# Kernel tuning notes

Measured on AMD Instinct MI355X. Metric: run time of the kernel, lower is better.

Reference implementation:

```python
import jax, jax.numpy as jnp
import numpy as np

B, D, H, K, V, M = 64, 4096, 32, 128, 128, 4096


def setup_inputs() -> dict:
    key = jax.random.key(0)
    ks = jax.random.split(key, 7)
    return {
        "x": jax.random.normal(ks[0], (B, D), dtype=jnp.float32),
        "prev_K": jax.random.normal(ks[1], (B, M, K), dtype=jnp.float32),
        "prev_V": jax.random.normal(ks[2], (B, M, V), dtype=jnp.float32),
        "P_q": jax.random.normal(ks[3], (H, D, K), dtype=jnp.float32),
        "P_k": jax.random.normal(ks[4], (D, K), dtype=jnp.float32),
        "P_v": jax.random.normal(ks[5], (D, V), dtype=jnp.float32),
        "P_o": jax.random.normal(ks[6], (H, D, V), dtype=jnp.float32),
    }


def reference(x, prev_K, prev_V, P_q, P_k, P_v, P_o):
    # Per-head query projection: [b,d] x [h,d,k] -> [b,h,k]
    q = jnp.einsum('bd,hdk->bhk', x, P_q)
    # Single shared K/V head (multi-query): append new token to cache along m
    new_k = jnp.einsum('bd,dk->bk', x, P_k)  # [b,k]
    new_v = jnp.einsum('bd,dv->bv', x, P_v)  # [b,v]
    Kc = jnp.concatenate([prev_K, new_k[:, None, :]], axis=1)  # [b,m+1,k]
    Vc = jnp.concatenate([prev_V, new_v[:, None, :]], axis=1)  # [b,m+1,v]
    # Attention over cache
    logits = jnp.einsum('bhk,bmk->bhm', q, Kc)
    weights = jax.nn.softmax(logits, axis=-1)
    O = jnp.einsum('bhm,bmv->bhv', weights, Vc)
    # Output projection: [b,h,v] x [h,d,v] -> [b,d]
    y = jnp.einsum('bhv,hdv->bd', O, P_o)
    return (y, Kc, Vc)
```

## Files before the change

### kernel.cpp

```cpp
#include <hip/hip_runtime.h>
#include <math.h>

#define Bb 64
#define Dd 4096
#define Hh 32
#define Kk 128
#define Vv 128
#define Mm 4096
#define MC 4097
#define NCH 16
#define NSLOT 17

#define WS_K1P  0
#define WS_Q    4456448
#define WS_NEWK (WS_Q + Bb*Hh*Kk)
#define WS_NEWV (WS_NEWK + Bb*Kk)
#define WS_PM   (WS_NEWV + Bb*Vv)
#define WS_PL   (WS_PM + Bb*NSLOT*Hh)
#define WS_PO   (WS_PL + Bb*NSLOT*Hh)
#define WS_O    (WS_PO + Bb*NSLOT*Hh*Vv)
#define WS_YP   (WS_O + Bb*Hh*Vv)

#define YSLOT (Bb*Dd)

#define OUT_Y  0
#define OUT_KC (Bb*Dd)
#define OUT_VC (OUT_KC + Bb*MC*Kk)

__global__ __launch_bounds__(256) void k1A_proj(const float* __restrict__ x,
        const float* __restrict__ Pq, const float* __restrict__ Pk,
        const float* __restrict__ Pv, float* __restrict__ part) {
    const int hidx = blockIdx.x;
    const int d0c  = blockIdx.y * 256;
    const int t = threadIdx.x;
    const int kg = t & 15, bg = t >> 4;
    const int kd = kg * 4, b0 = bg * 4;

    const float* P;
    if (hidx < Hh)       P = Pq + (size_t)hidx * Dd * Kk;
    else if (hidx == Hh) P = Pk;
    else                 P = Pv;

    __shared__ float xs[32 * 65];
    __shared__ float ps[32 * 128];

    float acc[4][8];
    #pragma unroll
    for (int a = 0; a < 4; a++)
        #pragma unroll
        for (int c = 0; c < 8; c++) acc[a][c] = 0.f;

    for (int tt = 0; tt < 8; tt++) {
        const int d0 = d0c + tt * 32;
        #pragma unroll
        for (int ii = 0; ii < 8; ii++) {
            int f = ii * 256 + t;
            int i = f & 31, bb = f >> 5;
            xs[i * 65 + bb] = x[(size_t)bb * Dd + d0 + i];
        }
        #pragma unroll
        for (int ii = 0; ii < 4; ii++) {
            int f = ii * 256 + t;
            int i = f >> 5, k4 = (f & 31) * 4;
            *(float4*)&ps[i * 128 + k4] = *(const float4*)&P[(size_t)(d0 + i) * Kk + k4];
        }
        __syncthreads();
        #pragma unroll
        for (int i = 0; i < 32; i++) {
            float xb[4];
            #pragma unroll
            for (int a = 0; a < 4; a++) xb[a] = xs[i * 65 + b0 + a];
            float4 p0 = *(float4*)&ps[i * 128 + kd];
            float4 p1 = *(float4*)&ps[i * 128 + 64 + kd];
            float pp[8] = {p0.x, p0.y, p0.z, p0.w, p1.x, p1.y, p1.z, p1.w};
            #pragma unroll
            for (int a = 0; a < 4; a++)
                #pragma unroll
                for (int c = 0; c < 8; c++)
                    acc[a][c] = fmaf(xb[a], pp[c], acc[a][c]);
        }
        __syncthreads();
    }
    float* dst = part + ((size_t)hidx * 16 + blockIdx.y) * 8192;
    #pragma unroll
    for (int a = 0; a < 4; a++) {
        int b = b0 + a;
        *(float4*)&dst[b * 128 + kd]      = make_float4(acc[a][0], acc[a][1], acc[a][2], acc[a][3]);
        *(float4*)&dst[b * 128 + 64 + kd] = make_float4(acc[a][4], acc[a][5], acc[a][6], acc[a][7]);
    }
}

__global__ __launch_bounds__(256) void k1B_reduce(const float* __restrict__ part,
        float* __restrict__ ws) {
    const int o = blockIdx.x * 256 + threadIdx.x;
    const int hidx = o >> 13;
    const int rest = o & 8191;
    float s = 0.f;
    #pragma unroll
    for (int c = 0; c < 16; c++) s += part[((size_t)hidx * 16 + c) * 8192 + rest];
    if (hidx < Hh) {
        int b = rest >> 7, k = rest & 127;
        ws[WS_Q + ((size_t)b * Hh + hidx) * Kk + k] = s;
    } else if (hidx == Hh) {
        ws[WS_NEWK + rest] = s;
    } else {
        ws[WS_NEWV + rest] = s;
    }
}

__global__ __launch_bounds__(256) void kflash(const float* __restrict__ prevK,
        const float* __restrict__ prevV, const float* __restrict__ wq,
        float* __restrict__ outKc, float* __restrict__ outVc,
        float* __restrict__ PM, float* __restrict__ PL, float* __restrict__ PO) {
    const int c = blockIdx.x;
    const int b = blockIdx.y;
    const int t = threadIdx.x;
    const int hg = t >> 4, lg = t & 15;
    const int h2 = hg * 2;

    __shared__ float ks_t[64 * 64];
    __shared__ float vs[64 * 132];
    __shared__ float qs[128 * 34];
    __shared__ float wl_t[64 * 36];

    {
        const int h = t >> 3, kc = t & 7;
        const float* qr = wq + ((size_t)b * Hh + h) * Kk + kc * 16;
        float4 a0 = *(const float4*)&qr[0];
        float4 a1 = *(const float4*)&qr[4];
        float4 a2 = *(const float4*)&qr[8];
        float4 a3 = *(const float4*)&qr[12];
        const int k0 = kc * 16;
        qs[(k0+ 0)*34 + h] = a0.x; qs[(k0+ 1)*34 + h] = a0.y;
        qs[(k0+ 2)*34 + h] = a0.z; qs[(k0+ 3)*34 + h] = a0.w;
        qs[(k0+ 4)*34 + h] = a1.x; qs[(k0+ 5)*34 + h] = a1.y;
        qs[(k0+ 6)*34 + h] = a1.z; qs[(k0+ 7)*34 + h] = a1.w;
        qs[(k0+ 8)*34 + h] = a2.x; qs[(k0+ 9)*34 + h] = a2.y;
        qs[(k0+10)*34 + h] = a2.z; qs[(k0+11)*34 + h] = a2.w;
        qs[(k0+12)*34 + h] = a3.x; qs[(k0+13)*34 + h] = a3.y;
        qs[(k0+14)*34 + h] = a3.z; qs[(k0+15)*34 + h] = a3.w;
    }

    float rm[2] = {-3.0e38f, -3.0e38f};
    float rl[2] = {0.f, 0.f};
    float accO[2][8] = {};
    const int kq = t & 15;
    const int vq = t & 31;

    for (int st = 0; st < 4; st++) {
        const int m0 = c * 256 + st * 64;
        __syncthreads();
        float4 kreg[8], vreg[8];
        #pragma unroll
        for (int ii = 0; ii < 4; ii++) {
            int mm = (t >> 4) + ii * 16;
            const float* src = prevK + ((size_t)b * Mm + m0 + mm) * Kk + kq * 4;
            kreg[ii]     = *(const float4*)src;
            kreg[ii + 4] = *(const float4*)(src + 64);
        }
        #pragma unroll
        for (int ii = 0; ii < 8; ii++) {
            int mm = (t >> 5) + ii * 8;
            vreg[ii] = *(const float4*)(prevV + ((size_t)b * Mm + m0 + mm) * Vv + vq * 4);
        }
        #pragma unroll
        for (int ii = 0; ii < 4; ii++) {
            int mm = (t >> 4) + ii * 16;
            int cs = (mm + 4 * kq) & 63;
            ks_t[(kq*4+0)*64 + cs] = kreg[ii].x;
            ks_t[(kq*4+1)*64 + cs] = kreg[ii].y;
            ks_t[(kq*4+2)*64 + cs] = kreg[ii].z;
            ks_t[(kq*4+3)*64 + cs] = kreg[ii].w;
        }
        #pragma unroll
        for (int ii = 0; ii < 8; ii++) {
            int mm = (t >> 5) + ii * 8;
            *(float4*)&vs[mm * 132 + vq * 4] = vreg[ii];
        }
        __syncthreads();
        #pragma unroll
        for (int ii = 0; ii < 4; ii++) {
            int mm = (t >> 4) + ii * 16;
            float* dstK = outKc + ((size_t)b * MC + m0 + mm) * Kk + kq * 4;
            *(float4*)dstK        = kreg[ii];
            *(float4*)(dstK + 64) = kreg[ii + 4];
        }
        #pragma unroll
        for (int ii = 0; ii < 8; ii++) {
            int mm = (t >> 5) + ii * 8;
            *(float4*)(outVc + ((size_t)b * MC + m0 + mm) * Vv + vq * 4) = vreg[ii];
        }
        float s[2][4] = {};
        #pragma unroll 4
        for (int k = 0; k < 64; k++) {
            float2 q2 = *(float2*)&qs[k * 34 + h2];
            float4 k4 = *(float4*)&ks_t[k * 64 + ((4*lg + 4*(k>>2)) & 63)];
            s[0][0] = fmaf(q2.x, k4.x, s[0][0]); s[0][1] = fmaf(q2.x, k4.y, s[0][1]);
            s[0][2] = fmaf(q2.x, k4.z, s[0][2]); s[0][3] = fmaf(q2.x, k4.w, s[0][3]);
            s[1][0] = fmaf(q2.y, k4.x, s[1][0]); s[1][1] = fmaf(q2.y, k4.y, s[1][1]);
            s[1][2] = fmaf(q2.y, k4.z, s[1][2]); s[1][3] = fmaf(q2.y, k4.w, s[1][3]);
        }
        __syncthreads();
        #pragma unroll
        for (int ii = 0; ii < 4; ii++) {
            int mm = (t >> 4) + ii * 16;
            int cs = (mm + 4 * kq) & 63;
            ks_t[(kq*4+0)*64 + cs] = kreg[ii+4].x;
            ks_t[(kq*4+1)*64 + cs] = kreg[ii+4].y;
            ks_t[(kq*4+2)*64 + cs] = kreg[ii+4].z;
            ks_t[(kq*4+3)*64 + cs] = kreg[ii+4].w;
        }
        __syncthreads();
        #pragma unroll 4
        for (int k = 0; k < 64; k++) {
            float2 q2 = *(float2*)&qs[(64 + k) * 34 + h2];
            float4 k4 = *(float4*)&ks_t[k * 64 + ((4*lg + 4*(k>>2)) & 63)];
            s[0][0] = fmaf(q2.x, k4.x, s[0][0]); s[0][1] = fmaf(q2.x, k4.y, s[0][1]);
            s[0][2] = fmaf(q2.x, k4.z, s[0][2]); s[0][3] = fmaf(q2.x, k4.w, s[0][3]);
            s[1][0] = fmaf(q2.y, k4.x, s[1][0]); s[1][1] = fmaf(q2.y, k4.y, s[1][1]);
            s[1][2] = fmaf(q2.y, k4.z, s[1][2]); s[1][3] = fmaf(q2.y, k4.w, s[1][3]);
        }
        float al[2];
        #pragma unroll
        for (int a = 0; a < 2; a++) {
            float mloc = fmaxf(fmaxf(s[a][0], s[a][1]), fmaxf(s[a][2], s[a][3]));
            mloc = fmaxf(mloc, __shfl_xor(mloc, 1, 64));
            mloc = fmaxf(mloc, __shfl_xor(mloc, 2, 64));
            mloc = fmaxf(mloc, __shfl_xor(mloc, 4, 64));
            mloc = fmaxf(mloc, __shfl_xor(mloc, 8, 64));
            float nm = fmaxf(rm[a], mloc);
            al[a] = __expf(rm[a] - nm);
            float psum = 0.f;
            #pragma unroll
            for (int cc = 0; cc < 4; cc++) {
                float p = __expf(s[a][cc] - nm);
                wl_t[(4*lg + cc) * 36 + h2 + a] = p;
                psum += p;
            }
            psum += __shfl_xor(psum, 1, 64);
            psum += __shfl_xor(psum, 2, 64);
            psum += __shfl_xor(psum, 4, 64);
            psum += __shfl_xor(psum, 8, 64);
            rl[a] = rl[a] * al[a] + psum;
            rm[a] = nm;
        }
        #pragma unroll
        for (int a = 0; a < 2; a++)
            #pragma unroll
            for (int j = 0; j < 8; j++) accO[a][j] *= al[a];
        for (int mm = 0; mm < 64; mm++) {
            float2 w2 = *(float2*)&wl_t[mm * 36 + h2];
            float4 v0 = *(float4*)&vs[mm * 132 + 4 * lg];
            float4 v1 = *(float4*)&vs[mm * 132 + 64 + 4 * lg];
            accO[0][0] = fmaf(w2.x, v0.x, accO[0][0]);
            accO[0][1] = fmaf(w2.x, v0.y, accO[0][1]);
            accO[0][2] = fmaf(w2.x, v0.z, accO[0][2]);
            accO[0][3] = fmaf(w2.x, v0.w, accO[0][3]);
            accO[0][4] = fmaf(w2.x, v1.x, accO[0][4]);
            accO[0][5] = fmaf(w2.x, v1.y, accO[0][5]);
            accO[0][6] = fmaf(w2.x, v1.z, accO[0][6]);
            accO[0][7] = fmaf(w2.x, v1.w, accO[0][7]);
            accO[1][0] = fmaf(w2.y, v0.x, accO[1][0]);
            accO[1][1] = fmaf(w2.y, v0.y, accO[1][1]);
            accO[1][2] = fmaf(w2.y, v0.z, accO[1][2]);
            accO[1][3] = fmaf(w2.y, v0.w, accO[1][3]);
            accO[1][4] = fmaf(w2.y, v1.x, accO[1][4]);
            accO[1][5] = fmaf(w2.y, v1.y, accO[1][5]);
            accO[1][6] = fmaf(w2.y, v1.z, accO[1][6]);
            accO[1][7] = fmaf(w2.y, v1.w, accO[1][7]);
        }
    }
    const size_t base = ((size_t)b * NSLOT + c) * Hh;
    if (lg == 0) {
        PM[base + h2]     = rm[0];
        PM[base + h2 + 1] = rm[1];
        PL[base + h2]     = rl[0];
        PL[base + h2 + 1] = rl[1];
    }
    #pragma unroll
    for (int a = 0; a < 2; a++) {
        float* po = PO + (base + h2 + a) * Vv;
        *(float4*)&po[4*lg]      = make_float4(accO[a][0], accO[a][1], accO[a][2], accO[a][3]);
        *(float4*)&po[64 + 4*lg] = make_float4(accO[a][4], accO[a][5], accO[a][6], accO[a][7]);
    }
}

__global__ __launch_bounds__(128) void knew(const float* __restrict__ ws,
        float* __restrict__ outKc, float* __restrict__ outVc,
        float* __restrict__ PM, float* __restrict__ PL, float* __restrict__ PO) {
    const int b = blockIdx.x, t = threadIdx.x;
    const float* q    = ws + WS_Q;
    const float* newk = ws + WS_NEWK;
    const float* newv = ws + WS_NEWV;
    const int h = t >> 2, j = t & 3;
    const float* qr = q + ((size_t)b * Hh + h) * Kk + j * 32;
    const float* nk = newk + (size_t)b * Kk + j * 32;
    float s0 = 0.f, s1 = 0.f, s2 = 0.f, s3 = 0.f;
    #pragma unroll
    for (int i = 0; i < 8; i++) {
        float4 a  = *(const float4*)&qr[i * 4];
        float4 c4 = *(const float4*)&nk[i * 4];
        s0 = fmaf(a.x, c4.x, s0); s1 = fmaf(a.y, c4.y, s1);
        s2 = fmaf(a.z, c4.z, s2); s3 = fmaf(a.w, c4.w, s3);
    }
    float s = (s0 + s1) + (s2 + s3);
    s += __shfl_xor(s, 1, 64);
    s += __shfl_xor(s, 2, 64);
    const size_t base = ((size_t)b * NSLOT + 16) * Hh;
    if (j == 0) { PM[base + h] = s; PL[base + h] = 1.f; }
    float nv = newv[(size_t)b * Vv + t];
    outKc[((size_t)b * MC + Mm) * Kk + t] = newk[(size_t)b * Kk + t];
    outVc[((size_t)b * MC + Mm) * Vv + t] = nv;
    #pragma unroll 4
    for (int hh = 0; hh < Hh; hh++)
        PO[(base + hh) * Vv + t] = nv;
}

__global__ __launch_bounds__(128) void kcomb(const float* __restrict__ PM,
        const float* __restrict__ PL, const float* __restrict__ PO,
        float* __restrict__ O) {
    const int h = blockIdx.x, b = blockIdx.y, t = threadIdx.x;
    __shared__ float ml[NSLOT], ll[NSLOT];
    if (t < NSLOT) {
        ml[t] = PM[((size_t)b * NSLOT + t) * Hh + h];
        ll[t] = PL[((size_t)b * NSLOT + t) * Hh + h];
    }
    __syncthreads();
    float M = -3.0e38f;
    #pragma unroll
    for (int c = 0; c < NSLOT; c++) M = fmaxf(M, ml[c]);
    float L = 0.f, o = 0.f;
    #pragma unroll
    for (int c = 0; c < NSLOT; c++) {
        float e = __expf(ml[c] - M);
        L += ll[c] * e;
        o = fmaf(e, PO[(((size_t)b * NSLOT + c) * Hh + h) * Vv + t], o);
    }
    O[((size_t)b * Hh + h) * Vv + t] = o / L;
}

__global__ __launch_bounds__(256) void k5_outproj(const float* __restrict__ O,
        const float* __restrict__ Po, float* __restrict__ ypart) {
    const int dbase = blockIdx.x * 64;
    const int hq = blockIdx.y;
    const int t = threadIdx.x;
    __shared__ float os[64 * 64];
    __shared__ float ps2[64 * 64];
    const int dg = t & 15, bg = t >> 4;
    const int d0 = dg * 4, b0 = bg * 4;
    float acc[4][4] = {};
    for (int hi = 0; hi < 4; hi++) {
        const int h = hq * 4 + hi;
        for (int vh = 0; vh < 2; vh++) {
            __syncthreads();
            #pragma unroll
            for (int ii = 0; ii < 4; ii++) {
                int f = ii * 256 + t;
                int vq2 = f & 15, r = f >> 4;
                int colp = (4 * vq2 + 4 * (r >> 2)) & 63;
                *(float4*)&os[r * 64 + colp] =
                    *(const float4*)&O[((size_t)(r * Hh + h)) * Vv + vh * 64 + 4 * vq2];
                *(float4*)&ps2[r * 64 + colp] =
                    *(const float4*)&Po[((size_t)h * Dd + dbase + r) * Vv + vh * 64 + 4 * vq2];
            }
            __syncthreads();
            #pragma unroll
            for (int v4 = 0; v4 < 16; v4++) {
                float4 pd[4], ob[4];
                #pragma unroll
                for (int cc = 0; cc < 4; cc++)
                    pd[cc] = *(float4*)&ps2[(d0 + cc) * 64 + ((4*v4 + 4*dg) & 63)];
                #pragma unroll
                for (int a = 0; a < 4; a++)
                    ob[a] = *(float4*)&os[(b0 + a) * 64 + ((4*v4 + 4*bg) & 63)];
                #pragma unroll
                for (int a = 0; a < 4; a++)
                    #pragma unroll
                    for (int cc = 0; cc < 4; cc++) {
                        acc[a][cc] = fmaf(ob[a].x, pd[cc].x, acc[a][cc]);
                        acc[a][cc] = fmaf(ob[a].y, pd[cc].y, acc[a][cc]);
                        acc[a][cc] = fmaf(ob[a].z, pd[cc].z, acc[a][cc]);
                        acc[a][cc] = fmaf(ob[a].w, pd[cc].w, acc[a][cc]);
                    }
            }
        }
    }
    float* yp = ypart + (size_t)hq * YSLOT;
    #pragma unroll
    for (int a = 0; a < 4; a++)
        *(float4*)&yp[(size_t)(b0 + a) * Dd + dbase + d0] =
            make_float4(acc[a][0], acc[a][1], acc[a][2], acc[a][3]);
}

__global__ __launch_bounds__(256) void k5r_yreduce(const float* __restrict__ ypart,
        float* __restrict__ y) {
    const int o = blockIdx.x * 256 + threadIdx.x;
    float s = 0.f;
    #pragma unroll
    for (int c = 0; c < 8; c++) s += ypart[(size_t)c * YSLOT + o];
    y[o] = s;
}

extern "C" void kernel_launch(void* const* d_in, const int* in_sizes, int n_in,
                              void* d_out, int out_size, void* d_ws, size_t ws_size,
                              hipStream_t stream) {
    const float* x     = (const float*)d_in[0];
    const float* prevK = (const float*)d_in[1];
    const float* prevV = (const float*)d_in[2];
    const float* Pq    = (const float*)d_in[3];
    const float* Pk    = (const float*)d_in[4];
    const float* Pv    = (const float*)d_in[5];
    const float* Po    = (const float*)d_in[6];
    float* out = (float*)d_out;
    float* ws  = (float*)d_ws;

    k1A_proj<<<dim3(Hh + 2, 16), 256, 0, stream>>>(x, Pq, Pk, Pv, ws + WS_K1P);
    k1B_reduce<<<(34 * 8192) / 256, 256, 0, stream>>>(ws + WS_K1P, ws);
    kflash<<<dim3(NCH, Bb), 256, 0, stream>>>(prevK, prevV, ws + WS_Q,
                                              out + OUT_KC, out + OUT_VC,
                                              ws + WS_PM, ws + WS_PL, ws + WS_PO);
    knew<<<Bb, 128, 0, stream>>>(ws, out + OUT_KC, out + OUT_VC,
                                 ws + WS_PM, ws + WS_PL, ws + WS_PO);
    kcomb<<<dim3(Hh, Bb), 128, 0, stream>>>(ws + WS_PM, ws + WS_PL, ws + WS_PO,
                                            ws + WS_O);
    k5_outproj<<<dim3(64, 8), 256, 0, stream>>>(ws + WS_O, Po, ws + WS_YP);
    k5r_yreduce<<<YSLOT / 256, 256, 0, stream>>>(ws + WS_YP, out + OUT_Y);
}
```

Measured before the change: 252.9 us.

## Halve LDS footprint in flash kernel to raise occupancy, stage Q from registers

```diff
diff --git a/kernel.cpp b/kernel.cpp
--- a/kernel.cpp
+++ b/kernel.cpp
@@ -27,6 +27,13 @@
 #define OUT_KC (Bb*Dd)
 #define OUT_VC (OUT_KC + Bb*MC*Kk)
 
+#define BAR_LGKM() do { \
+    __builtin_amdgcn_sched_barrier(0); \
+    asm volatile("s_waitcnt lgkmcnt(0)" ::: "memory"); \
+    __builtin_amdgcn_s_barrier(); \
+    __builtin_amdgcn_sched_barrier(0); \
+} while (0)
+
 __global__ __launch_bounds__(256) void k1A_proj(const float* __restrict__ x,
         const float* __restrict__ Pq, const float* __restrict__ Pk,
         const float* __restrict__ Pv, float* __restrict__ part) {
@@ -108,7 +115,7 @@
     }
 }
 
-__global__ __launch_bounds__(256) void kflash(const float* __restrict__ prevK,
+__global__ __launch_bounds__(256, 3) void kflash(const float* __restrict__ prevK,
         const float* __restrict__ prevV, const float* __restrict__ wq,
         float* __restrict__ outKc, float* __restrict__ outVc,
         float* __restrict__ PM, float* __restrict__ PL, float* __restrict__ PO) {
@@ -117,80 +124,76 @@
     const int t = threadIdx.x;
     const int hg = t >> 4, lg = t & 15;
     const int h2 = hg * 2;
+    const int kq = t & 15;
+    const int mK = t >> 4;
+    const int vq = t & 31;
+    const int mV = t >> 5;
 
     __shared__ float ks_t[64 * 64];
-    __shared__ float vs[64 * 132];
-    __shared__ float qs[128 * 34];
+    __shared__ float vs[32 * 132];
+    __shared__ float qs[64 * 34];
     __shared__ float wl_t[64 * 36];
 
-    {
-        const int h = t >> 3, kc = t & 7;
-        const float* qr = wq + ((size_t)b * Hh + h) * Kk + kc * 16;
-        float4 a0 = *(const float4*)&qr[0];
-        float4 a1 = *(const float4*)&qr[4];
-        float4 a2 = *(const float4*)&qr[8];
-        float4 a3 = *(const float4*)&qr[12];
-        const int k0 = kc * 16;
-        qs[(k0+ 0)*34 + h] = a0.x; qs[(k0+ 1)*34 + h] = a0.y;
-        qs[(k0+ 2)*34 + h] = a0.z; qs[(k0+ 3)*34 + h] = a0.w;
-        qs[(k0+ 4)*34 + h] = a1.x; qs[(k0+ 5)*34 + h] = a1.y;
-        qs[(k0+ 6)*34 + h] = a1.z; qs[(k0+ 7)*34 + h] = a1.w;
-        qs[(k0+ 8)*34 + h] = a2.x; qs[(k0+ 9)*34 + h] = a2.y;
-        qs[(k0+10)*34 + h] = a2.z; qs[(k0+11)*34 + h] = a2.w;
-        qs[(k0+12)*34 + h] = a3.x; qs[(k0+13)*34 + h] = a3.y;
-        qs[(k0+14)*34 + h] = a3.z; qs[(k0+15)*34 + h] = a3.w;
-    }
+    float4 qreg[2][2];
+    #pragma unroll
+    for (int hf = 0; hf < 2; hf++)
+        #pragma unroll
+        for (int a = 0; a < 2; a++)
+            qreg[hf][a] = *(const float4*)&wq[((size_t)b * Hh + h2 + a) * Kk + hf * 64 + lg * 4];
 
     float rm[2] = {-3.0e38f, -3.0e38f};
     float rl[2] = {0.f, 0.f};
     float accO[2][8] = {};
-    const int kq = t & 15;
-    const int vq = t & 31;
 
     for (int st = 0; st < 4; st++) {
         const int m0 = c * 256 + st * 64;
-        __syncthreads();
-        float4 kreg[8], vreg[8];
+        BAR_LGKM();
+        float4 ka[8], va[8];
         #pragma unroll
         for (int ii = 0; ii < 4; ii++) {
-            int mm = (t >> 4) + ii * 16;
+            int mm = mK + ii * 16;
             const float* src = prevK + ((size_t)b * Mm + m0 + mm) * Kk + kq * 4;
-            kreg[ii]     = *(const float4*)src;
-            kreg[ii + 4] = *(const float4*)(src + 64);
+            ka[ii]     = *(const float4*)src;
+            ka[ii + 4] = *(const float4*)(src + 64);
         }
         #pragma unroll
         for (int ii = 0; ii < 8; ii++) {
-            int mm = (t >> 5) + ii * 8;
-            vreg[ii] = *(const float4*)(prevV + ((size_t)b * Mm + m0 + mm) * Vv + vq * 4);
-        }
+            int mm = mV + ii * 8;
+            va[ii] = *(const float4*)(prevV + ((size_t)b * Mm + m0 + mm) * Vv + vq * 4);
+        }
+        #pragma unroll
+        for (int ii = 0; ii < 4; ii++)
+            *(float4*)&vs[(mV + ii * 8) * 132 + vq * 4] = va[ii];
         #pragma unroll
         for (int ii = 0; ii < 4; ii++) {
-            int mm = (t >> 4) + ii * 16;
+            int mm = mK + ii * 16;
             int cs = (mm + 4 * kq) & 63;
-            ks_t[(kq*4+0)*64 + cs] = kreg[ii].x;
-            ks_t[(kq*4+1)*64 + cs] = kreg[ii].y;
-            ks_t[(kq*4+2)*64 + cs] = kreg[ii].z;
-            ks_t[(kq*4+3)*64 + cs] = kreg[ii].w;
+            ks_t[(kq*4+0)*64 + cs] = ka[ii].x;
+            ks_t[(kq*4+1)*64 + cs] = ka[ii].y;
+            ks_t[(kq*4+2)*64 + cs] = ka[ii].z;
+            ks_t[(kq*4+3)*64 + cs] = ka[ii].w;
+        }
+        {
+            float q0[4] = {qreg[0][0].x, qreg[0][0].y, qreg[0][0].z, qreg[0][0].w};
+            float q1[4] = {qreg[0][1].x, qreg[0][1].y, qreg[0][1].z, qreg[0][1].w};
+            #pragma unroll
+            for (int j = 0; j < 4; j++)
+                *(float2*)&qs[(lg * 4 + j) * 34 + h2] = make_float2(q0[j], q1[j]);
+        }
+        BAR_LGKM();
+        #pragma unroll
+        for (int ii = 0; ii < 4; ii++) {
+            int mm = mK + ii * 16;
+            float* dK = outKc + ((size_t)b * MC + m0 + mm) * Kk + kq * 4;
+            *(float4*)dK        = ka[ii];
+            *(float4*)(dK + 64) = ka[ii + 4];
         }
         #pragma unroll
         for (int ii = 0; ii < 8; ii++) {
-            int mm = (t >> 5) + ii * 8;
-            *(float4*)&vs[mm * 132 + vq * 4] = vreg[ii];
-        }
-        __syncthreads();
-        #pragma unroll
-        for (int ii = 0; ii < 4; ii++) {
-            int mm = (t >> 4) + ii * 16;
-            float* dstK = outKc + ((size_t)b * MC + m0 + mm) * Kk + kq * 4;
-            *(float4*)dstK        = kreg[ii];
-            *(float4*)(dstK + 64) = kreg[ii + 4];
-        }
-        #pragma unroll
-        for (int ii = 0; ii < 8; ii++) {
-            int mm = (t >> 5) + ii * 8;
-            *(float4*)(outVc + ((size_t)b * MC + m0 + mm) * Vv + vq * 4) = vreg[ii];
-        }
-        float s[2][4] = {};
+            int mm = mV + ii * 8;
+            *(float4*)(outVc + ((size_t)b * MC + m0 + mm) * Vv + vq * 4) = va[ii];
+        }
+        float s[2][4] = {{0.f,0.f,0.f,0.f},{0.f,0.f,0.f,0.f}};
         #pragma unroll 4
         for (int k = 0; k < 64; k++) {
             float2 q2 = *(float2*)&qs[k * 34 + h2];
@@ -200,20 +203,27 @@
             s[1][0] = fmaf(q2.y, k4.x, s[1][0]); s[1][1] = fmaf(q2.y, k4.y, s[1][1]);
             s[1][2] = fmaf(q2.y, k4.z, s[1][2]); s[1][3] = fmaf(q2.y, k4.w, s[1][3]);
         }
-        __syncthreads();
+        BAR_LGKM();
         #pragma unroll
         for (int ii = 0; ii < 4; ii++) {
-            int mm = (t >> 4) + ii * 16;
+            int mm = mK + ii * 16;
             int cs = (mm + 4 * kq) & 63;
-            ks_t[(kq*4+0)*64 + cs] = kreg[ii+4].x;
-            ks_t[(kq*4+1)*64 + cs] = kreg[ii+4].y;
-            ks_t[(kq*4+2)*64 + cs] = kreg[ii+4].z;
-            ks_t[(kq*4+3)*64 + cs] = kreg[ii+4].w;
-        }
-        __syncthreads();
+            ks_t[(kq*4+0)*64 + cs] = ka[ii+4].x;
+            ks_t[(kq*4+1)*64 + cs] = ka[ii+4].y;
+            ks_t[(kq*4+2)*64 + cs] = ka[ii+4].z;
+            ks_t[(kq*4+3)*64 + cs] = ka[ii+4].w;
+        }
+        {
+            float q0[4] = {qreg[1][0].x, qreg[1][0].y, qreg[1][0].z, qreg[1][0].w};
+            float q1[4] = {qreg[1][1].x, qreg[1][1].y, qreg[1][1].z, qreg[1][1].w};
+            #pragma unroll
+            for (int j = 0; j < 4; j++)
+                *(float2*)&qs[(lg * 4 + j) * 34 + h2] = make_float2(q0[j], q1[j]);
+        }
+        BAR_LGKM();
         #pragma unroll 4
         for (int k = 0; k < 64; k++) {
-            float2 q2 = *(float2*)&qs[(64 + k) * 34 + h2];
+            float2 q2 = *(float2*)&qs[k * 34 + h2];
             float4 k4 = *(float4*)&ks_t[k * 64 + ((4*lg + 4*(k>>2)) & 63)];
             s[0][0] = fmaf(q2.x, k4.x, s[0][0]); s[0][1] = fmaf(q2.x, k4.y, s[0][1]);
             s[0][2] = fmaf(q2.x, k4.z, s[0][2]); s[0][3] = fmaf(q2.x, k4.w, s[0][3]);
@@ -248,7 +258,8 @@
         for (int a = 0; a < 2; a++)
             #pragma unroll
             for (int j = 0; j < 8; j++) accO[a][j] *= al[a];
-        for (int mm = 0; mm < 64; mm++) {
+        #pragma unroll 4
+        for (int mm = 0; mm < 32; mm++) {
             float2 w2 = *(float2*)&wl_t[mm * 36 + h2];
             float4 v0 = *(float4*)&vs[mm * 132 + 4 * lg];
             float4 v1 = *(float4*)&vs[mm * 132 + 64 + 4 * lg];
@@ -269,6 +280,33 @@
             accO[1][6] = fmaf(w2.y, v1.z, accO[1][6]);
             accO[1][7] = fmaf(w2.y, v1.w, accO[1][7]);
         }
+        BAR_LGKM();
+        #pragma unroll
+        for (int ii = 0; ii < 4; ii++)
+            *(float4*)&vs[(mV + ii * 8) * 132 + vq * 4] = va[ii + 4];
+        BAR_LGKM();
+        #pragma unroll 4
+        for (int mm = 0; mm < 32; mm++) {
+            float2 w2 = *(float2*)&wl_t[(32 + mm) * 36 + h2];
+            float4 v0 = *(float4*)&vs[mm * 132 + 4 * lg];
+            float4 v1 = *(float4*)&vs[mm * 132 + 64 + 4 * lg];
+            accO[0][0] = fmaf(w2.x, v0.x, accO[0][0]);
+            accO[0][1] = fmaf(w2.x, v0.y, accO[0][1]);
+            accO[0][2] = fmaf(w2.x, v0.z, accO[0][2]);
+            accO[0][3] = fmaf(w2.x, v0.w, accO[0][3]);
+            accO[0][4] = fmaf(w2.x, v1.x, accO[0][4]);
+            accO[0][5] = fmaf(w2.x, v1.y, accO[0][5]);
+            accO[0][6] = fmaf(w2.x, v1.z, accO[0][6]);
+            accO[0][7] = fmaf(w2.x, v1.w, accO[0][7]);
+            accO[1][0] = fmaf(w2.y, v0.x, accO[1][0]);
+            accO[1][1] = fmaf(w2.y, v0.y, accO[1][1]);
+            accO[1][2] = fmaf(w2.y, v0.z, accO[1][2]);
+            accO[1][3] = fmaf(w2.y, v0.w, accO[1][3]);
+            accO[1][4] = fmaf(w2.y, v1.x, accO[1][4]);
+            accO[1][5] = fmaf(w2.y, v1.y, accO[1][5]);
+            accO[1][6] = fmaf(w2.y, v1.z, accO[1][6]);
+            accO[1][7] = fmaf(w2.y, v1.w, accO[1][7]);
+        }
     }
     const size_t base = ((size_t)b * NSLOT + c) * Hh;
     if (lg == 0) {
@@ -306,7 +344,7 @@
     float s = (s0 + s1) + (s2 + s3);
     s += __shfl_xor(s, 1, 64);
     s += __shfl_xor(s, 2, 64);
-    const size_t base = ((size_t)b * NSLOT + 16) * Hh;
+    const size_t base = ((size_t)b * NSLOT + NCH) * Hh;
     if (j == 0) { PM[base + h] = s; PL[base + h] = 1.f; }
     float nv = newv[(size_t)b * Vv + t];
     outKc[((size_t)b * MC + Mm) * Kk + t] = newk[(size_t)b * Kk + t];
```

Result: slower. 325.8 us (+28.9%).
